# Optimization experiments

Measured on AMD Instinct MI355X. Metric: run time of the kernel, lower is better.

## Reference

```python
import jax, jax.numpy as jnp
import numpy as np

INF = 1.0e7   # matches torch INF = 1.0 * 10000000.0
EOS_ID = 2
FIN_INIT = -1.0e9  # finite stand-in for torch's -inf init of fin_log_probs


def setup_inputs() -> dict:
    key = jax.random.key(0)
    k1, k2, k3, k4, k5, k6 = jax.random.split(key, 6)
    P, D, S, V = 32, 8, 2048, 128000
    # next-token probability distribution per (prompt, draft)
    logits = jax.random.normal(k1, (P * D, V), dtype=jnp.float32)
    probs = jax.nn.softmax(logits, axis=-1)
    alive_seq = jax.random.randint(k2, (P, D, S), 0, V, dtype=jnp.int32)
    fin_seq = jax.random.randint(k3, (P, D, S), 0, V, dtype=jnp.int32)
    alive_log_probs = -5.0 * jax.random.uniform(k4, (P, D), dtype=jnp.float32)
    fin_log_probs = jnp.full((P, D), FIN_INIT, dtype=jnp.float32)
    still_prompt = jax.random.randint(k5, (P,), 0, 2) == 1
    is_first = jax.random.randint(k6, (P,), 0, 2) == 1
    return {"probs": probs, "alive_seq": alive_seq, "fin_seq": fin_seq,
            "alive_log_probs": alive_log_probs, "fin_log_probs": fin_log_probs,
            "still_prompt": still_prompt, "is_first": is_first, "cur_pos": 1024}


def reference(probs, alive_seq, fin_seq, alive_log_probs, fin_log_probs,
              still_prompt, is_first, cur_pos):
    P, D = alive_log_probs.shape
    V = probs.shape[-1]
    # log-prob accumulation (smoothing=None path)
    log_probs = jnp.log(probs.reshape(P, D, V))                  # (P, D, V)
    curr = alive_log_probs[:, :, None] + log_probs               # (P, D, V)
    # joint topk over beams*vocab
    flat = curr.reshape(P, D * V)
    topk_lp, topk_i = jax.lax.top_k(flat, 2 * D)                 # (P, 2D)
    topk_beam_id = topk_i // V
    topk_tok = topk_i % V
    # first-generation override: only beam 0 counts
    f_vals, f_idx = jax.lax.top_k(log_probs[:, 0, :], 2 * D)     # (P, 2D)
    m = is_first[:, None]
    topk_tok = jnp.where(m, f_idx, topk_tok)
    topk_lp = jnp.where(m, alive_log_probs[:, 0:1] + f_vals, topk_lp)
    # gather parent sequences, write new token at cur_pos
    topk_seq = jnp.take_along_axis(alive_seq, topk_beam_id[:, :, None], axis=1)
    topk_seq = topk_seq.at[:, :, cur_pos].set(topk_tok)
    topk_finished = topk_tok == EOS_ID
    # grow_alive: keep best unfinished
    alive_masked = topk_lp + topk_finished * (-INF)
    na_lp, na_idx = jax.lax.top_k(alive_masked, D)               # (P, D)
    na_seq = jnp.take_along_axis(topk_seq, na_idx[:, :, None], axis=1)
    attention_change_ids = jnp.take_along_axis(topk_beam_id, na_idx, axis=1)
    # grow_fin: keep best finished among old + new
    fin_masked = topk_lp + (~topk_finished) * (-INF)
    cat_seq = jnp.concatenate([fin_seq, topk_seq], axis=1)       # (P, 3D, S)
    cat_lp = jnp.concatenate([fin_log_probs, fin_masked], axis=1)
    nf_lp, nf_idx = jax.lax.top_k(cat_lp, D)
    nf_seq = jnp.take_along_axis(cat_seq, nf_idx[:, :, None], axis=1)
    # still-prompt masking: keep old state, identity attention ids
    sp = still_prompt
    attention_change_ids = jnp.where(sp[:, None], jnp.arange(D), attention_change_ids)
    new_alive_seq = jnp.where(sp[:, None, None], alive_seq, na_seq)
    new_alive_lp = jnp.where(sp[:, None], alive_log_probs, na_lp)
    new_fin_seq = jnp.where(sp[:, None, None], fin_seq, nf_seq)
    new_fin_lp = jnp.where(sp[:, None], fin_log_probs, nf_lp)
    return (attention_change_ids, new_alive_seq, new_alive_lp, new_fin_seq, new_fin_lp)
```

## Files before the change

### kernel.cpp

```cpp
#include <hip/hip_runtime.h>
#include <stdint.h>

#define NEG_BIG -3.0e38f
#define INF_ 10000000.0f
#define EOS_ID 2
#define V_DIM 128000
#define S_DIM 2048
#define CAP 4096
#define SEG_ELEMS 32000

__device__ __forceinline__ bool better(float v1, int i1, float v2, int i2) {
    return (v1 > v2) || (v1 == v2 && i1 < i2);
}
__device__ __forceinline__ float bf16_up(uint16_t u) {
    return __uint_as_float(((uint32_t)u) << 16);
}

__device__ __forceinline__ void hist_b16(uint4 q, int etop, unsigned long long& c0) {
    uint32_t wd[4] = {q.x, q.y, q.z, q.w};
    #pragma unroll
    for (int c = 0; c < 4; ++c) {
        int e0 = (int)((wd[c] >> 7) & 0xFF);
        int e1 = (int)(wd[c] >> 23);
        int k0 = etop - e0; k0 = k0 < 0 ? 0 : (k0 > 7 ? 7 : k0);
        int k1 = etop - e1; k1 = k1 < 0 ? 0 : (k1 > 7 ? 7 : k1);
        c0 += 1ull << (k0 << 3);
        c0 += 1ull << (k1 << 3);
    }
}
__device__ __forceinline__ void hist_f32u(uint4 q, int etop, unsigned long long& c0) {
    uint32_t u[4] = {q.x, q.y, q.z, q.w};
    #pragma unroll
    for (int c = 0; c < 4; ++c) {
        int e = (int)(u[c] >> 23);
        int k = etop - e; k = k < 0 ? 0 : (k > 7 ? 7 : k);
        c0 += 1ull << (k << 3);
    }
}

__global__ __launch_bounds__(512, 8) void rowtopk_kernel(const void* probs,
    const uint32_t* finlp, float* s1_val, int* s1_idx) {
    const int r = blockIdx.x >> 2;
    const int h = blockIdx.x & 3;
    const int t = threadIdx.x;
    const int wave = t >> 6, lane = t & 63;
    const bool isbf16 = (finlp[0] == 0xCE6ECE6Eu);

    __shared__ int s_etop, s_B, s_ncand;
    __shared__ uint32_t s_part[8][4];
    __shared__ uint32_t s_bins[8];
    __shared__ uint32_t s_wmax[8];
    __shared__ uint32_t s_cv[CAP];
    __shared__ int s_ci[CAP];

    const uint4* segb = (const uint4*)((const uint16_t*)probs + (size_t)r * V_DIM) + h * 4000;
    const uint4* segu = (const uint4*)((const float*)probs + (size_t)r * V_DIM) + h * 8000;
    const int idxbase = h * SEG_ELEMS;

    uint4 q0, q1, q2, q3;
    if (isbf16) {
        q0 = segb[t];          q1 = segb[512 + t];
        q2 = make_uint4(0,0,0,0); q3 = make_uint4(0,0,0,0);
    } else {
        q0 = segu[t];          q1 = segu[512 + t];
        q2 = segu[1024 + t];   q3 = segu[1536 + t];
    }

    uint32_t m = 0;
    if (isbf16) {
        #define MB(q) { uint32_t w[4]={(q).x,(q).y,(q).z,(q).w};                 \
            _Pragma("unroll")                                                    \
            for (int c = 0; c < 4; ++c) {                                        \
                uint32_t lo = w[c] << 16, hi = w[c] & 0xFFFF0000u;               \
                m = lo > m ? lo : m; m = hi > m ? hi : m; } }
        MB(q0) MB(q1)
        #undef MB
    } else {
        #define MF(q) { uint32_t w[4]={(q).x,(q).y,(q).z,(q).w};                 \
            _Pragma("unroll")                                                    \
            for (int c = 0; c < 4; ++c) { m = w[c] > m ? w[c] : m; } }
        MF(q0) MF(q1) MF(q2) MF(q3)
        #undef MF
    }
    #pragma unroll
    for (int s = 1; s < 64; s <<= 1) {
        uint32_t o = (uint32_t)__shfl_xor((int)m, s, 64);
        m = o > m ? o : m;
    }
    if (lane == 0) s_wmax[wave] = m;
    __syncthreads();
    if (t == 0) {
        uint32_t mm = 0;
        for (int w = 0; w < 8; ++w) mm = s_wmax[w] > mm ? s_wmax[w] : mm;
        int ea = (int)(mm >> 23);
        s_etop = ea + 1 > 254 ? 254 : ea + 1;
    }
    __syncthreads();

    for (int attempt = 0; attempt < 6; ++attempt) {
        if (t < 32) ((uint32_t*)s_part)[t] = 0;
        if (t == 0) s_B = -1;
        __syncthreads();
        const int etop = s_etop;
        unsigned long long c0 = 0;
        if (isbf16) {
            hist_b16(q0, etop, c0); hist_b16(q1, etop, c0);
        } else {
            hist_f32u(q0, etop, c0); hist_f32u(q1, etop, c0);
            hist_f32u(q2, etop, c0); hist_f32u(q3, etop, c0);
        }
        uint32_t f0 = (uint32_t)(c0 & 0xFF)         | (((uint32_t)(c0 >> 8)  & 0xFF) << 16);
        uint32_t f1 = ((uint32_t)(c0 >> 16) & 0xFF) | (((uint32_t)(c0 >> 24) & 0xFF) << 16);
        uint32_t f2 = ((uint32_t)(c0 >> 32) & 0xFF) | (((uint32_t)(c0 >> 40) & 0xFF) << 16);
        uint32_t f3 = ((uint32_t)(c0 >> 48) & 0xFF) | (((uint32_t)(c0 >> 56) & 0xFF) << 16);
        #pragma unroll
        for (int s = 1; s < 64; s <<= 1) {
            f0 += (uint32_t)__shfl_xor((int)f0, s, 64);
            f1 += (uint32_t)__shfl_xor((int)f1, s, 64);
            f2 += (uint32_t)__shfl_xor((int)f2, s, 64);
            f3 += (uint32_t)__shfl_xor((int)f3, s, 64);
        }
        if (lane == 0) {
            s_part[wave][0] = f0; s_part[wave][1] = f1;
            s_part[wave][2] = f2; s_part[wave][3] = f3;
        }
        __syncthreads();
        if (t < 8) {
            uint32_t s = 0;
            for (int w = 0; w < 8; ++w)
                s += (s_part[w][t >> 1] >> ((t & 1) * 16)) & 0xFFFFu;
            s_bins[t] = s;
        }
        __syncthreads();
        if (t == 0) {
            uint32_t cum = 0; int B = -1;
            for (int b = 0; b < 7; ++b) {
                cum += s_bins[b];
                if (cum >= 16) { B = b; break; }
            }
            if (B >= 0) s_B = B; else s_etop = etop - 7;
        }
        __syncthreads();
        if (s_B >= 0) break;
    }

    if (t == 0) s_ncand = 0;
    __syncthreads();
    const int Bsel = (s_B >= 0) ? s_B : 6;
    int ethr = s_etop - Bsel; if (ethr < 0) ethr = 0;
    const uint32_t thr = (uint32_t)ethr << 23;

    #define FILT_B(qv, basepos)                                                 \
    {   uint32_t wd[4] = {(qv).x, (qv).y, (qv).z, (qv).w};                      \
        _Pragma("unroll")                                                       \
        for (int c = 0; c < 4; ++c) {                                           \
            uint32_t lo = wd[c] << 16;                                          \
            uint32_t hi = wd[c] & 0xFFFF0000u;                                  \
            if (lo >= thr) {                                                    \
                int slot = atomicAdd(&s_ncand, 1);                              \
                if (slot < CAP) { s_cv[slot] = lo; s_ci[slot] = idxbase + (basepos) * 8 + c * 2; } \
            }                                                                   \
            if (hi >= thr) {                                                    \
                int slot = atomicAdd(&s_ncand, 1);                              \
                if (slot < CAP) { s_cv[slot] = hi; s_ci[slot] = idxbase + (basepos) * 8 + c * 2 + 1; } \
            }                                                                   \
        }                                                                       \
    }
    #define FILT_FU(qv, basepos)                                                \
    {   uint32_t u[4] = {(qv).x, (qv).y, (qv).z, (qv).w};                       \
        _Pragma("unroll")                                                       \
        for (int c = 0; c < 4; ++c) {                                           \
            if (u[c] >= thr) {                                                  \
                int slot = atomicAdd(&s_ncand, 1);                              \
                if (slot < CAP) { s_cv[slot] = u[c]; s_ci[slot] = idxbase + (basepos) * 4 + c; } \
            }                                                                   \
        }                                                                       \
    }

    if (isbf16) {
        FILT_B(q0, t); FILT_B(q1, 512 + t);
        {
            uint4 a0 = segb[1024 + t];
            uint4 a1 = segb[1536 + t];
            uint4 a2 = segb[2048 + t];
            uint4 a3 = segb[2560 + t];
            FILT_B(a0, 1024 + t); FILT_B(a1, 1536 + t);
            FILT_B(a2, 2048 + t); FILT_B(a3, 2560 + t);
        }
        {
            uint4 a0 = segb[3072 + t];
            FILT_B(a0, 3072 + t);
            if (t < 416) { uint4 a1 = segb[3584 + t]; FILT_B(a1, 3584 + t); }
        }
    } else {
        FILT_FU(q0, t);          FILT_FU(q1, 512 + t);
        FILT_FU(q2, 1024 + t);   FILT_FU(q3, 1536 + t);
        #pragma unroll
        for (int g = 0; g < 2; ++g) {
            const int base = 2048 + g * 2048;
            uint4 a0 = segu[base + t];
            uint4 a1 = segu[base + 512 + t];
            uint4 a2 = segu[base + 1024 + t];
            uint4 a3 = segu[base + 1536 + t];
            FILT_FU(a0, base + t);        FILT_FU(a1, base + 512 + t);
            FILT_FU(a2, base + 1024 + t); FILT_FU(a3, base + 1536 + t);
        }
        {
            uint4 a0 = segu[6144 + t];
            uint4 a1 = segu[6656 + t];
            uint4 a2 = segu[7168 + t];
            FILT_FU(a0, 6144 + t); FILT_FU(a1, 6656 + t); FILT_FU(a2, 7168 + t);
            if (t < 320) { uint4 a3 = segu[7680 + t]; FILT_FU(a3, 7680 + t); }
        }
    }
    __syncthreads();
    const int C = s_ncand < CAP ? s_ncand : CAP;

    if (t < 64) {
        unsigned long long taken = 0;
        for (int k = 0; k < 16; ++k) {
            float bv = NEG_BIG; int bi = 0x7fffffff; int bs = -1;
            int q = 0;
            for (int j = lane; j < C; j += 64, ++q) {
                if ((taken >> q) & 1ull) continue;
                float v = __uint_as_float(s_cv[j]);
                int ix = s_ci[j];
                if (better(v, ix, bv, bi)) { bv = v; bi = ix; bs = j; }
            }
            #pragma unroll
            for (int mm = 1; mm < 64; mm <<= 1) {
                float ov = __shfl_xor(bv, mm, 64);
                int oi = __shfl_xor(bi, mm, 64);
                int os = __shfl_xor(bs, mm, 64);
                if (better(ov, oi, bv, bi)) { bv = ov; bi = oi; bs = os; }
            }
            if (bs >= 0 && (bs & 63) == lane) taken |= 1ull << (bs >> 6);
            if (lane == 0) {
                s1_val[(r * 4 + h) * 16 + k] = bv;
                s1_idx[(r * 4 + h) * 16 + k] = bi;
            }
        }
    }
}

__global__ __launch_bounds__(64) void merge_kernel(const float* s1_val,
    const int* s1_idx, float* ws_val, int* ws_idx) {
    const int r = blockIdx.x;
    const int lane = threadIdx.x;
    float v = s1_val[r * 64 + lane];
    int ix = s1_idx[r * 64 + lane];
    bool taken = false;
    for (int k = 0; k < 16; ++k) {
        float bv = taken ? NEG_BIG : v;
        int bi = taken ? 0x7fffffff : ix;
        int bj = lane;
        #pragma unroll
        for (int m = 1; m < 64; m <<= 1) {
            float ov = __shfl_xor(bv, m, 64);
            int oi = __shfl_xor(bi, m, 64);
            int oj = __shfl_xor(bj, m, 64);
            if (better(ov, oi, bv, bi)) { bv = ov; bi = oi; bj = oj; }
        }
        if (bj == lane) taken = true;
        if (lane == 0) { ws_val[r * 16 + k] = bv; ws_idx[r * 16 + k] = bi; }
    }
}

__global__ __launch_bounds__(256) void selcopy_kernel(
    const void* alive_lp_p, const void* fin_lp_p,
    const int* alive_seq, const int* fin_seq,
    const uint32_t* spw, const uint32_t* isfw, const int* cur_pos_p,
    const float* ws_val, const int* ws_idx, float* out) {
    const int bi = blockIdx.x;
    const int arr = bi >> 8;
    const int rk = bi & 255;
    const int p = rk >> 3, kk = rk & 7;
    const int t = threadIdx.x;
    const int lane = t & 63;

    __shared__ float cv[128]; __shared__ int cflat[128];
    __shared__ float s_alive_lp[8]; __shared__ float s_fin_lp[8];
    __shared__ float topk_lp[16]; __shared__ int topk_tok[16]; __shared__ int topk_beam[16];
    __shared__ int na_sel[8]; __shared__ float na_val[8];
    __shared__ int nf_sel[8]; __shared__ float nf_val[8];
    __shared__ int s_src, s_patch;

    const bool isbf16 = (((const uint32_t*)fin_lp_p)[0] == 0xCE6ECE6Eu);
    uint32_t w1 = (lane < 8) ? spw[lane] : 0u;
    uint32_t w2 = (lane < 8) ? isfw[lane] : 0u;
    const bool bbyte = (__ballot(w1 > 1u || w2 > 1u) != 0ull);

    const bool sp  = bbyte ? (((const uint8_t*)spw)[p] != 0) : (spw[p] != 0u);
    const bool isf = bbyte ? (((const uint8_t*)isfw)[p] != 0) : (isfw[p] != 0u);

    if (t < 8) {
        float a, f;
        if (isbf16) {
            a = bf16_up(((const uint16_t*)alive_lp_p)[p * 8 + t]);
            f = bf16_up(((const uint16_t*)fin_lp_p)[p * 8 + t]);
        } else {
            a = ((const float*)alive_lp_p)[p * 8 + t];
            f = ((const float*)fin_lp_p)[p * 8 + t];
        }
        s_alive_lp[t] = a; s_fin_lp[t] = f;
    }
    __syncthreads();

    if (t < 128) {
        int d = t >> 4, m = t & 15;
        int r = p * 8 + d;
        cv[t] = s_alive_lp[d] + logf(ws_val[r * 16 + m]);
        cflat[t] = d * V_DIM + ws_idx[r * 16 + m];
    }
    __syncthreads();

    if (t < 64) {
        bool taken0 = false, taken1 = false;
        for (int k = 0; k < 16; ++k) {
            float v0 = taken0 ? NEG_BIG : cv[lane];
            int   f0 = taken0 ? 0x7fffffff : cflat[lane];
            float v1 = taken1 ? NEG_BIG : cv[lane + 64];
            int   f1 = taken1 ? 0x7fffffff : cflat[lane + 64];
            float bv; int bf, bj;
            if (better(v0, f0, v1, f1)) { bv = v0; bf = f0; bj = lane; }
            else                        { bv = v1; bf = f1; bj = lane + 64; }
            #pragma unroll
            for (int m = 1; m < 64; m <<= 1) {
                float ov = __shfl_xor(bv, m, 64);
                int   of = __shfl_xor(bf, m, 64);
                int   oj = __shfl_xor(bj, m, 64);
                if (better(ov, of, bv, bf)) { bv = ov; bf = of; bj = oj; }
            }
            if (bj == lane)      taken0 = true;
            if (bj == lane + 64) taken1 = true;
            if (lane == 0) {
                topk_lp[k]   = bv;
                topk_beam[k] = bf / V_DIM;
                topk_tok[k]  = bf % V_DIM;
            }
        }
    }
    __syncthreads();

    if (isf && t < 16) {
        int r0 = p * 8;
        topk_tok[t] = ws_idx[r0 * 16 + t];
        topk_lp[t]  = s_alive_lp[0] + logf(ws_val[r0 * 16 + t]);
    }
    __syncthreads();

    if (t < 64) {
        {
            float mv = NEG_BIG; int mi = 0x7fffffff;
            if (lane < 16) {
                mv = topk_lp[lane] + ((topk_tok[lane] == EOS_ID) ? -INF_ : 0.0f);
                mi = lane;
            }
            bool taken = false;
            for (int k = 0; k < 8; ++k) {
                float bv = taken ? NEG_BIG : mv;
                int   bix = taken ? 0x7fffffff : mi;
                #pragma unroll
                for (int m = 1; m < 64; m <<= 1) {
                    float ov = __shfl_xor(bv, m, 64);
                    int   oi = __shfl_xor(bix, m, 64);
                    if (better(ov, oi, bv, bix)) { bv = ov; bix = oi; }
                }
                if (lane < 16 && bix == mi) taken = true;
                if (lane == 0) { na_sel[k] = bix; na_val[k] = bv; }
            }
        }
        {
            float fv = NEG_BIG; int fi = 0x7fffffff;
            if (lane < 8) { fv = s_fin_lp[lane]; fi = lane; }
            else if (lane < 24) {
                int j = lane - 8;
                fv = topk_lp[j] + ((topk_tok[j] == EOS_ID) ? 0.0f : -INF_);
                fi = lane;
            }
            bool taken = false;
            for (int k = 0; k < 8; ++k) {
                float bv = taken ? NEG_BIG : fv;
                int   bix = taken ? 0x7fffffff : fi;
                #pragma unroll
                for (int m = 1; m < 64; m <<= 1) {
                    float ov = __shfl_xor(bv, m, 64);
                    int   oi = __shfl_xor(bix, m, 64);
                    if (better(ov, oi, bv, bix)) { bv = ov; bix = oi; }
                }
                if (lane < 24 && bix == fi) taken = true;
                if (lane == 0) { nf_sel[k] = bix; nf_val[k] = bv; }
            }
        }
    }
    __syncthreads();

    float* out_attn = out;
    float* out_alp  = out + 256 + 524288;
    float* out_flp  = out + 512 + 2 * 524288;
    if (t == 0) {
        int na = na_sel[kk], nf = nf_sel[kk];
        if (arr == 0) {
            out_attn[p * 8 + kk] = (float)(sp ? kk : topk_beam[na]);
            out_alp[p * 8 + kk]  = sp ? s_alive_lp[kk] : na_val[kk];
            out_flp[p * 8 + kk]  = sp ? s_fin_lp[kk]   : nf_val[kk];
        }
        int src, patch;
        if (arr == 0) {
            if (sp) { src = p * 8 + kk; patch = -1; }
            else    { src = p * 8 + topk_beam[na]; patch = topk_tok[na]; }
        } else {
            if (sp) { src = (p * 8 + kk) | (1 << 30); patch = -1; }
            else if (nf < 8) { src = (p * 8 + nf) | (1 << 30); patch = -1; }
            else { int j = nf - 8; src = p * 8 + topk_beam[j]; patch = topk_tok[j]; }
        }
        s_src = src; s_patch = patch;
    }
    __syncthreads();

    const int src = s_src, patch = s_patch;
    const int* s = ((src >> 30) & 1) ? fin_seq : alive_seq;
    const int4* srow = (const int4*)(s + (size_t)(src & 0x3FFFFFFF) * S_DIM);
    float* drow = out + (arr ? (512 + 524288) : 256) + (size_t)rk * S_DIM;
    const int cp = cur_pos_p[0];

    for (int i = t; i < S_DIM / 4; i += 256) {
        int4 v = srow[i];
        if (patch >= 0) {
            int s0 = i * 4;
            if (s0 + 0 == cp) v.x = patch;
            if (s0 + 1 == cp) v.y = patch;
            if (s0 + 2 == cp) v.z = patch;
            if (s0 + 3 == cp) v.w = patch;
        }
        ((float4*)drow)[i] = make_float4((float)v.x, (float)v.y, (float)v.z, (float)v.w);
    }
}

extern "C" void kernel_launch(void* const* d_in, const int* in_sizes, int n_in,
                              void* d_out, int out_size, void* d_ws, size_t ws_size,
                              hipStream_t stream) {
    (void)in_sizes; (void)n_in; (void)out_size; (void)ws_size;
    const void* probs      = d_in[0];
    const int*  alive_seq  = (const int*)d_in[1];
    const int*  fin_seq    = (const int*)d_in[2];
    const void* alive_lp   = d_in[3];
    const void* fin_lp     = d_in[4];
    const uint32_t* spw    = (const uint32_t*)d_in[5];
    const uint32_t* isfw   = (const uint32_t*)d_in[6];
    const int*  cur_pos    = (const int*)d_in[7];

    float* ws_val = (float*)d_ws;
    int*   ws_idx = (int*)((char*)d_ws + 16384);

    float* s1_val = (float*)d_out + 256;
    int*   s1_idx = (int*)((float*)d_out + 256 + 16384);

    rowtopk_kernel<<<1024, 512, 0, stream>>>(probs, (const uint32_t*)fin_lp, s1_val, s1_idx);
    merge_kernel<<<256, 64, 0, stream>>>(s1_val, s1_idx, ws_val, ws_idx);
    selcopy_kernel<<<512, 256, 0, stream>>>(alive_lp, fin_lp, alive_seq, fin_seq,
                                            spw, isfw, cur_pos, ws_val, ws_idx,
                                            (float*)d_out);
}
```

Measured before the change: 246.6 us.

## Split row top-k into eighths with threshold-filter passes replacing exponent histogram

The row top-k kernel now splits each vocab row into 8 segments of 256 threads instead of 4 segments of 512. The exponent-histogram threshold search over register-held data is replaced by a multi-pass scheme: set a threshold from the first-chunk max, stream the whole segment filtering candidates into shared memory, and adjust the threshold and re-stream if the count falls outside [16, CAP]. A brute-force 16-pass fallback handles failure. The merge kernel now takes 128 partial candidates per row. The aim is more parallelism and less histogram work, at the cost of possible re-reads of global memory when the first threshold misses.

```diff
diff --git a/kernel.cpp b/kernel.cpp
--- a/kernel.cpp
+++ b/kernel.cpp
@@ -6,263 +6,247 @@
 #define EOS_ID 2
 #define V_DIM 128000
 #define S_DIM 2048
-#define CAP 4096
-#define SEG_ELEMS 32000
+#define CAP 2048
+#define SEG_ELEMS 16000
 
 __device__ __forceinline__ bool better(float v1, int i1, float v2, int i2) {
     return (v1 > v2) || (v1 == v2 && i1 < i2);
 }
+__device__ __forceinline__ bool betteru(uint32_t v1, int i1, uint32_t v2, int i2) {
+    return (v1 > v2) || (v1 == v2 && i1 < i2);
+}
 __device__ __forceinline__ float bf16_up(uint16_t u) {
     return __uint_as_float(((uint32_t)u) << 16);
 }
 
-__device__ __forceinline__ void hist_b16(uint4 q, int etop, unsigned long long& c0) {
-    uint32_t wd[4] = {q.x, q.y, q.z, q.w};
-    #pragma unroll
-    for (int c = 0; c < 4; ++c) {
-        int e0 = (int)((wd[c] >> 7) & 0xFF);
-        int e1 = (int)(wd[c] >> 23);
-        int k0 = etop - e0; k0 = k0 < 0 ? 0 : (k0 > 7 ? 7 : k0);
-        int k1 = etop - e1; k1 = k1 < 0 ? 0 : (k1 > 7 ? 7 : k1);
-        c0 += 1ull << (k0 << 3);
-        c0 += 1ull << (k1 << 3);
-    }
-}
-__device__ __forceinline__ void hist_f32u(uint4 q, int etop, unsigned long long& c0) {
-    uint32_t u[4] = {q.x, q.y, q.z, q.w};
-    #pragma unroll
-    for (int c = 0; c < 4; ++c) {
-        int e = (int)(u[c] >> 23);
-        int k = etop - e; k = k < 0 ? 0 : (k > 7 ? 7 : k);
-        c0 += 1ull << (k << 3);
-    }
-}
-
-__global__ __launch_bounds__(512, 8) void rowtopk_kernel(const void* probs,
+__global__ __launch_bounds__(256, 8) void rowtopk_kernel(const void* probs,
     const uint32_t* finlp, float* s1_val, int* s1_idx) {
-    const int r = blockIdx.x >> 2;
-    const int h = blockIdx.x & 3;
+    const int r = blockIdx.x >> 3;
+    const int h = blockIdx.x & 7;
     const int t = threadIdx.x;
     const int wave = t >> 6, lane = t & 63;
     const bool isbf16 = (finlp[0] == 0xCE6ECE6Eu);
 
-    __shared__ int s_etop, s_B, s_ncand;
-    __shared__ uint32_t s_part[8][4];
-    __shared__ uint32_t s_bins[8];
-    __shared__ uint32_t s_wmax[8];
+    __shared__ int s_ncand;
+    __shared__ uint32_t s_thr;
+    __shared__ uint32_t s_max;
+    __shared__ int s_M, s_ref;
+    __shared__ uint32_t s_wred[4];
+    __shared__ int s_wredi[4];
+    __shared__ uint32_t s_lv; __shared__ int s_li;
     __shared__ uint32_t s_cv[CAP];
     __shared__ int s_ci[CAP];
 
-    const uint4* segb = (const uint4*)((const uint16_t*)probs + (size_t)r * V_DIM) + h * 4000;
-    const uint4* segu = (const uint4*)((const float*)probs + (size_t)r * V_DIM) + h * 8000;
+    const uint4* segb = (const uint4*)((const uint16_t*)probs + (size_t)r * V_DIM) + h * 2000;
+    const uint4* segu = (const uint4*)((const float*)probs + (size_t)r * V_DIM) + h * 4000;
     const int idxbase = h * SEG_ELEMS;
 
-    uint4 q0, q1, q2, q3;
+    uint32_t am = 0;
     if (isbf16) {
-        q0 = segb[t];          q1 = segb[512 + t];
-        q2 = make_uint4(0,0,0,0); q3 = make_uint4(0,0,0,0);
+        uint4 q = segb[t];
+        uint32_t w[4] = {q.x, q.y, q.z, q.w};
+        #pragma unroll
+        for (int c = 0; c < 4; ++c) {
+            uint32_t lo = w[c] << 16, hi = w[c] & 0xFFFF0000u;
+            am = lo > am ? lo : am; am = hi > am ? hi : am;
+        }
     } else {
-        q0 = segu[t];          q1 = segu[512 + t];
-        q2 = segu[1024 + t];   q3 = segu[1536 + t];
-    }
-
-    uint32_t m = 0;
-    if (isbf16) {
-        #define MB(q) { uint32_t w[4]={(q).x,(q).y,(q).z,(q).w};                 \
-            _Pragma("unroll")                                                    \
-            for (int c = 0; c < 4; ++c) {                                        \
-                uint32_t lo = w[c] << 16, hi = w[c] & 0xFFFF0000u;               \
-                m = lo > m ? lo : m; m = hi > m ? hi : m; } }
-        MB(q0) MB(q1)
-        #undef MB
-    } else {
-        #define MF(q) { uint32_t w[4]={(q).x,(q).y,(q).z,(q).w};                 \
-            _Pragma("unroll")                                                    \
-            for (int c = 0; c < 4; ++c) { m = w[c] > m ? w[c] : m; } }
-        MF(q0) MF(q1) MF(q2) MF(q3)
-        #undef MF
+        uint4 q = segu[t];
+        uint32_t w[4] = {q.x, q.y, q.z, q.w};
+        #pragma unroll
+        for (int c = 0; c < 4; ++c) am = w[c] > am ? w[c] : am;
     }
     #pragma unroll
     for (int s = 1; s < 64; s <<= 1) {
-        uint32_t o = (uint32_t)__shfl_xor((int)m, s, 64);
-        m = o > m ? o : m;
-    }
-    if (lane == 0) s_wmax[wave] = m;
+        uint32_t o = (uint32_t)__shfl_xor((int)am, s, 64);
+        am = o > am ? o : am;
+    }
+    if (lane == 0) s_wred[wave] = am;
     __syncthreads();
     if (t == 0) {
         uint32_t mm = 0;
-        for (int w = 0; w < 8; ++w) mm = s_wmax[w] > mm ? s_wmax[w] : mm;
-        int ea = (int)(mm >> 23);
-        s_etop = ea + 1 > 254 ? 254 : ea + 1;
-    }
-    __syncthreads();
-
-    for (int attempt = 0; attempt < 6; ++attempt) {
-        if (t < 32) ((uint32_t*)s_part)[t] = 0;
-        if (t == 0) s_B = -1;
-        __syncthreads();
-        const int etop = s_etop;
-        unsigned long long c0 = 0;
-        if (isbf16) {
-            hist_b16(q0, etop, c0); hist_b16(q1, etop, c0);
-        } else {
-            hist_f32u(q0, etop, c0); hist_f32u(q1, etop, c0);
-            hist_f32u(q2, etop, c0); hist_f32u(q3, etop, c0);
-        }
-        uint32_t f0 = (uint32_t)(c0 & 0xFF)         | (((uint32_t)(c0 >> 8)  & 0xFF) << 16);
-        uint32_t f1 = ((uint32_t)(c0 >> 16) & 0xFF) | (((uint32_t)(c0 >> 24) & 0xFF) << 16);
-        uint32_t f2 = ((uint32_t)(c0 >> 32) & 0xFF) | (((uint32_t)(c0 >> 40) & 0xFF) << 16);
-        uint32_t f3 = ((uint32_t)(c0 >> 48) & 0xFF) | (((uint32_t)(c0 >> 56) & 0xFF) << 16);
-        #pragma unroll
-        for (int s = 1; s < 64; s <<= 1) {
-            f0 += (uint32_t)__shfl_xor((int)f0, s, 64);
-            f1 += (uint32_t)__shfl_xor((int)f1, s, 64);
-            f2 += (uint32_t)__shfl_xor((int)f2, s, 64);
-            f3 += (uint32_t)__shfl_xor((int)f3, s, 64);
-        }
-        if (lane == 0) {
-            s_part[wave][0] = f0; s_part[wave][1] = f1;
-            s_part[wave][2] = f2; s_part[wave][3] = f3;
-        }
-        __syncthreads();
-        if (t < 8) {
-            uint32_t s = 0;
-            for (int w = 0; w < 8; ++w)
-                s += (s_part[w][t >> 1] >> ((t & 1) * 16)) & 0xFFFFu;
-            s_bins[t] = s;
-        }
-        __syncthreads();
-        if (t == 0) {
-            uint32_t cum = 0; int B = -1;
-            for (int b = 0; b < 7; ++b) {
-                cum += s_bins[b];
-                if (cum >= 16) { B = b; break; }
-            }
-            if (B >= 0) s_B = B; else s_etop = etop - 7;
-        }
-        __syncthreads();
-        if (s_B >= 0) break;
-    }
-
-    if (t == 0) s_ncand = 0;
-    __syncthreads();
-    const int Bsel = (s_B >= 0) ? s_B : 6;
-    int ethr = s_etop - Bsel; if (ethr < 0) ethr = 0;
-    const uint32_t thr = (uint32_t)ethr << 23;
-
+        for (int w = 0; w < 4; ++w) mm = s_wred[w] > mm ? s_wred[w] : mm;
+        s_thr = (mm >> 23) > 2 ? mm - 0x01000000u : 1u;
+        s_ref = 0; s_M = 2;
+    }
+    __syncthreads();
+
+    #define FILT_FU(qv, basepos)                                                \
+    {   uint32_t u0=(qv).x, u1=(qv).y, u2=(qv).z, u3=(qv).w;                    \
+        mx = u0 > mx ? u0 : mx; mx = u1 > mx ? u1 : mx;                         \
+        mx = u2 > mx ? u2 : mx; mx = u3 > mx ? u3 : mx;                         \
+        if (u0 >= thr) { int sl = atomicAdd(&s_ncand,1); if (sl<CAP){s_cv[sl]=u0; s_ci[sl]=idxbase+(basepos)*4+0;} } \
+        if (u1 >= thr) { int sl = atomicAdd(&s_ncand,1); if (sl<CAP){s_cv[sl]=u1; s_ci[sl]=idxbase+(basepos)*4+1;} } \
+        if (u2 >= thr) { int sl = atomicAdd(&s_ncand,1); if (sl<CAP){s_cv[sl]=u2; s_ci[sl]=idxbase+(basepos)*4+2;} } \
+        if (u3 >= thr) { int sl = atomicAdd(&s_ncand,1); if (sl<CAP){s_cv[sl]=u3; s_ci[sl]=idxbase+(basepos)*4+3;} } \
+    }
     #define FILT_B(qv, basepos)                                                 \
     {   uint32_t wd[4] = {(qv).x, (qv).y, (qv).z, (qv).w};                      \
         _Pragma("unroll")                                                       \
         for (int c = 0; c < 4; ++c) {                                           \
-            uint32_t lo = wd[c] << 16;                                          \
-            uint32_t hi = wd[c] & 0xFFFF0000u;                                  \
-            if (lo >= thr) {                                                    \
-                int slot = atomicAdd(&s_ncand, 1);                              \
-                if (slot < CAP) { s_cv[slot] = lo; s_ci[slot] = idxbase + (basepos) * 8 + c * 2; } \
-            }                                                                   \
-            if (hi >= thr) {                                                    \
-                int slot = atomicAdd(&s_ncand, 1);                              \
-                if (slot < CAP) { s_cv[slot] = hi; s_ci[slot] = idxbase + (basepos) * 8 + c * 2 + 1; } \
-            }                                                                   \
+            uint32_t lo = wd[c] << 16, hi = wd[c] & 0xFFFF0000u;                \
+            mx = lo > mx ? lo : mx; mx = hi > mx ? hi : mx;                     \
+            if (lo >= thr) { int sl = atomicAdd(&s_ncand,1); if (sl<CAP){s_cv[sl]=lo; s_ci[sl]=idxbase+(basepos)*8+c*2;} } \
+            if (hi >= thr) { int sl = atomicAdd(&s_ncand,1); if (sl<CAP){s_cv[sl]=hi; s_ci[sl]=idxbase+(basepos)*8+c*2+1;} } \
         }                                                                       \
     }
-    #define FILT_FU(qv, basepos)                                                \
-    {   uint32_t u[4] = {(qv).x, (qv).y, (qv).z, (qv).w};                       \
-        _Pragma("unroll")                                                       \
-        for (int c = 0; c < 4; ++c) {                                           \
-            if (u[c] >= thr) {                                                  \
-                int slot = atomicAdd(&s_ncand, 1);                              \
-                if (slot < CAP) { s_cv[slot] = u[c]; s_ci[slot] = idxbase + (basepos) * 4 + c; } \
-            }                                                                   \
-        }                                                                       \
-    }
-
-    if (isbf16) {
-        FILT_B(q0, t); FILT_B(q1, 512 + t);
-        {
-            uint4 a0 = segb[1024 + t];
-            uint4 a1 = segb[1536 + t];
-            uint4 a2 = segb[2048 + t];
-            uint4 a3 = segb[2560 + t];
-            FILT_B(a0, 1024 + t); FILT_B(a1, 1536 + t);
-            FILT_B(a2, 2048 + t); FILT_B(a3, 2560 + t);
-        }
-        {
-            uint4 a0 = segb[3072 + t];
-            FILT_B(a0, 3072 + t);
-            if (t < 416) { uint4 a1 = segb[3584 + t]; FILT_B(a1, 3584 + t); }
+
+    int C = 0;
+    bool ok = false;
+    for (int pass = 0; pass < 6 && !ok; ++pass) {
+        if (t == 0) s_ncand = 0;
+        __syncthreads();
+        const uint32_t thr = s_thr;
+        uint32_t mx = 0;
+        if (isbf16) {
+            uint4 a0 = segb[t],        a1 = segb[256 + t],  a2 = segb[512 + t];
+            uint4 a3 = segb[768 + t],  a4 = segb[1024 + t];
+            FILT_B(a0, t);        FILT_B(a1, 256 + t);  FILT_B(a2, 512 + t);
+            FILT_B(a3, 768 + t);  FILT_B(a4, 1024 + t);
+            a0 = segb[1280 + t];  a1 = segb[1536 + t];
+            FILT_B(a0, 1280 + t); FILT_B(a1, 1536 + t);
+            if (t < 208) { uint4 a5 = segb[1792 + t]; FILT_B(a5, 1792 + t); }
+        } else {
+            #pragma unroll
+            for (int g = 0; g < 3; ++g) {
+                const int base = g * 1280;
+                uint4 a0 = segu[base + t],        a1 = segu[base + 256 + t];
+                uint4 a2 = segu[base + 512 + t],  a3 = segu[base + 768 + t];
+                uint4 a4 = segu[base + 1024 + t];
+                FILT_FU(a0, base + t);        FILT_FU(a1, base + 256 + t);
+                FILT_FU(a2, base + 512 + t);  FILT_FU(a3, base + 768 + t);
+                FILT_FU(a4, base + 1024 + t);
+            }
+            if (t < 160) { uint4 a5 = segu[3840 + t]; FILT_FU(a5, 3840 + t); }
+        }
+        #pragma unroll
+        for (int s = 1; s < 64; s <<= 1) {
+            uint32_t o = (uint32_t)__shfl_xor((int)mx, s, 64);
+            mx = o > mx ? o : mx;
+        }
+        if (lane == 0) s_wred[wave] = mx;
+        __syncthreads();
+        if (t == 0) {
+            uint32_t mm = 0;
+            for (int w = 0; w < 4; ++w) mm = s_wred[w] > mm ? s_wred[w] : mm;
+            s_max = mm;
+        }
+        __syncthreads();
+        C = s_ncand;
+        ok = (C >= 16 && C <= CAP);
+        if (!ok && t == 0) {
+            int M;
+            if (s_ref == 0) { M = 2; s_ref = 1; }
+            else { M = (C > CAP) ? s_M - 1 : s_M + 2; }
+            M = M < 0 ? 0 : (M > 24 ? 24 : M);
+            s_M = M;
+            uint32_t e = s_max >> 23;
+            uint32_t Mm = e > (uint32_t)M ? (uint32_t)M : (e > 1 ? e - 1 : 0);
+            s_thr = s_max - (Mm << 23);
+        }
+        __syncthreads();
+    }
+
+    if (ok) {
+        if (t < 64) {
+            unsigned long long taken = 0;
+            for (int k = 0; k < 16; ++k) {
+                float bv = NEG_BIG; int bi = 0x7fffffff; int bs = -1;
+                int q = 0;
+                for (int j = lane; j < C; j += 64, ++q) {
+                    if ((taken >> q) & 1ull) continue;
+                    float v = __uint_as_float(s_cv[j]);
+                    int ix = s_ci[j];
+                    if (better(v, ix, bv, bi)) { bv = v; bi = ix; bs = j; }
+                }
+                #pragma unroll
+                for (int mm = 1; mm < 64; mm <<= 1) {
+                    float ov = __shfl_xor(bv, mm, 64);
+                    int oi = __shfl_xor(bi, mm, 64);
+                    int os = __shfl_xor(bs, mm, 64);
+                    if (better(ov, oi, bv, bi)) { bv = ov; bi = oi; bs = os; }
+                }
+                if (bs >= 0 && (bs & 63) == lane) taken |= 1ull << (bs >> 6);
+                if (lane == 0) {
+                    s1_val[(r * 8 + h) * 16 + k] = bv;
+                    s1_idx[(r * 8 + h) * 16 + k] = bi;
+                }
+            }
         }
     } else {
-        FILT_FU(q0, t);          FILT_FU(q1, 512 + t);
-        FILT_FU(q2, 1024 + t);   FILT_FU(q3, 1536 + t);
-        #pragma unroll
-        for (int g = 0; g < 2; ++g) {
-            const int base = 2048 + g * 2048;
-            uint4 a0 = segu[base + t];
-            uint4 a1 = segu[base + 512 + t];
-            uint4 a2 = segu[base + 1024 + t];
-            uint4 a3 = segu[base + 1536 + t];
-            FILT_FU(a0, base + t);        FILT_FU(a1, base + 512 + t);
-            FILT_FU(a2, base + 1024 + t); FILT_FU(a3, base + 1536 + t);
-        }
-        {
-            uint4 a0 = segu[6144 + t];
-            uint4 a1 = segu[6656 + t];
-            uint4 a2 = segu[7168 + t];
-            FILT_FU(a0, 6144 + t); FILT_FU(a1, 6656 + t); FILT_FU(a2, 7168 + t);
-            if (t < 320) { uint4 a3 = segu[7680 + t]; FILT_FU(a3, 7680 + t); }
-        }
-    }
-    __syncthreads();
-    const int C = s_ncand < CAP ? s_ncand : CAP;
-
-    if (t < 64) {
-        unsigned long long taken = 0;
+        uint32_t lv = 0xFFFFFFFFu; int li = -1;
         for (int k = 0; k < 16; ++k) {
-            float bv = NEG_BIG; int bi = 0x7fffffff; int bs = -1;
-            int q = 0;
-            for (int j = lane; j < C; j += 64, ++q) {
-                if ((taken >> q) & 1ull) continue;
-                float v = __uint_as_float(s_cv[j]);
-                int ix = s_ci[j];
-                if (better(v, ix, bv, bi)) { bv = v; bi = ix; bs = j; }
+            uint32_t bv = 0; int bi = 0x7fffffff;
+            if (isbf16) {
+                for (int pos = t; pos < 2000; pos += 256) {
+                    uint4 q = segb[pos];
+                    uint32_t wd[4] = {q.x, q.y, q.z, q.w};
+                    #pragma unroll
+                    for (int c = 0; c < 4; ++c) {
+                        uint32_t lo = wd[c] << 16, hi = wd[c] & 0xFFFF0000u;
+                        int i0 = idxbase + pos * 8 + c * 2, i1 = i0 + 1;
+                        if (betteru(lv, li, lo, i0) && betteru(lo, i0, bv, bi)) { bv = lo; bi = i0; }
+                        if (betteru(lv, li, hi, i1) && betteru(hi, i1, bv, bi)) { bv = hi; bi = i1; }
+                    }
+                }
+            } else {
+                for (int pos = t; pos < 4000; pos += 256) {
+                    uint4 q = segu[pos];
+                    uint32_t u[4] = {q.x, q.y, q.z, q.w};
+                    #pragma unroll
+                    for (int c = 0; c < 4; ++c) {
+                        int ix = idxbase + pos * 4 + c;
+                        if (betteru(lv, li, u[c], ix) && betteru(u[c], ix, bv, bi)) { bv = u[c]; bi = ix; }
+                    }
+                }
             }
             #pragma unroll
             for (int mm = 1; mm < 64; mm <<= 1) {
-                float ov = __shfl_xor(bv, mm, 64);
+                uint32_t ov = (uint32_t)__shfl_xor((int)bv, mm, 64);
                 int oi = __shfl_xor(bi, mm, 64);
-                int os = __shfl_xor(bs, mm, 64);
-                if (better(ov, oi, bv, bi)) { bv = ov; bi = oi; bs = os; }
-            }
-            if (bs >= 0 && (bs & 63) == lane) taken |= 1ull << (bs >> 6);
-            if (lane == 0) {
-                s1_val[(r * 4 + h) * 16 + k] = bv;
-                s1_idx[(r * 4 + h) * 16 + k] = bi;
-            }
-        }
-    }
+                if (betteru(ov, oi, bv, bi)) { bv = ov; bi = oi; }
+            }
+            if (lane == 0) { s_wred[wave] = bv; s_wredi[wave] = bi; }
+            __syncthreads();
+            if (t == 0) {
+                uint32_t wv = 0; int wi = 0x7fffffff;
+                for (int w = 0; w < 4; ++w)
+                    if (betteru(s_wred[w], s_wredi[w], wv, wi)) { wv = s_wred[w]; wi = s_wredi[w]; }
+                s_lv = wv; s_li = wi;
+                s1_val[(r * 8 + h) * 16 + k] = __uint_as_float(wv);
+                s1_idx[(r * 8 + h) * 16 + k] = wi;
+            }
+            __syncthreads();
+            lv = s_lv; li = s_li;
+        }
+    }
+    #undef FILT_FU
+    #undef FILT_B
 }
 
 __global__ __launch_bounds__(64) void merge_kernel(const float* s1_val,
     const int* s1_idx, float* ws_val, int* ws_idx) {
     const int r = blockIdx.x;
     const int lane = threadIdx.x;
-    float v = s1_val[r * 64 + lane];
-    int ix = s1_idx[r * 64 + lane];
-    bool taken = false;
+    float v0 = s1_val[r * 128 + lane];      int i0 = s1_idx[r * 128 + lane];
+    float v1 = s1_val[r * 128 + 64 + lane]; int i1 = s1_idx[r * 128 + 64 + lane];
+    bool tk0 = false, tk1 = false;
     for (int k = 0; k < 16; ++k) {
-        float bv = taken ? NEG_BIG : v;
-        int bi = taken ? 0x7fffffff : ix;
-        int bj = lane;
+        float a = tk0 ? NEG_BIG : v0; int ai = tk0 ? 0x7fffffff : i0;
+        float b = tk1 ? NEG_BIG : v1; int bi2 = tk1 ? 0x7fffffff : i1;
+        float bv; int bidx; int bj;
+        if (better(a, ai, b, bi2)) { bv = a; bidx = ai; bj = lane; }
+        else                       { bv = b; bidx = bi2; bj = lane + 64; }
         #pragma unroll
         for (int m = 1; m < 64; m <<= 1) {
             float ov = __shfl_xor(bv, m, 64);
-            int oi = __shfl_xor(bi, m, 64);
+            int oi = __shfl_xor(bidx, m, 64);
             int oj = __shfl_xor(bj, m, 64);
-            if (better(ov, oi, bv, bi)) { bv = ov; bi = oi; bj = oj; }
-        }
-        if (bj == lane) taken = true;
-        if (lane == 0) { ws_val[r * 16 + k] = bv; ws_idx[r * 16 + k] = bi; }
+            if (better(ov, oi, bv, bidx)) { bv = ov; bidx = oi; bj = oj; }
+        }
+        if (bj == lane)      tk0 = true;
+        if (bj == lane + 64) tk1 = true;
+        if (lane == 0) { ws_val[r * 16 + k] = bv; ws_idx[r * 16 + k] = bidx; }
     }
 }
 
@@ -454,9 +438,9 @@
     int*   ws_idx = (int*)((char*)d_ws + 16384);
 
     float* s1_val = (float*)d_out + 256;
-    int*   s1_idx = (int*)((float*)d_out + 256 + 16384);
-
-    rowtopk_kernel<<<1024, 512, 0, stream>>>(probs, (const uint32_t*)fin_lp, s1_val, s1_idx);
+    int*   s1_idx = (int*)((float*)d_out + 256 + 32768);
+
+    rowtopk_kernel<<<2048, 256, 0, stream>>>(probs, (const uint32_t*)fin_lp, s1_val, s1_idx);
     merge_kernel<<<256, 64, 0, stream>>>(s1_val, s1_idx, ws_val, ws_idx);
     selcopy_kernel<<<512, 256, 0, stream>>>(alive_lp, fin_lp, alive_seq, fin_seq,
                                             spw, isfw, cur_pos, ws_val, ws_idx,
```

New measurement: 405.9 us. 64.6% more time.
